# Kernel optimization log

Hardware: AMD Instinct MI355X
Metric: run time of the kernel (lower is better)

Reference implementation:

```python
import jax, jax.numpy as jnp
import numpy as np

W_BIJ, W_ORTH, W_LAP, W_PRE = 1000.0, 1000.0, 1.0, 100000.0
N, V, C, K = 8, 5000, 128, 128
NUM_DESC = int(C * 0.2)  # 25, matches sub_pre=0.2


def setup_inputs() -> dict:
    key = jax.random.key(0)
    ks = jax.random.split(key, 10)
    return {
        "C12": jax.random.normal(ks[0], (N, K, K), jnp.float32) * 0.1,
        "C21": jax.random.normal(ks[1], (N, K, K), jnp.float32) * 0.1,
        "feat_1": jax.random.normal(ks[2], (N, V, C), jnp.float32),
        "feat_2": jax.random.normal(ks[3], (N, V, C), jnp.float32),
        "evecs_1": jax.random.normal(ks[4], (N, V, K), jnp.float32) * 0.02,
        "evecs_2": jax.random.normal(ks[5], (N, V, K), jnp.float32) * 0.02,
        "evecs_trans1": jax.random.normal(ks[6], (N, K, V), jnp.float32) * 0.02,
        "evecs_trans2": jax.random.normal(ks[7], (N, K, V), jnp.float32) * 0.02,
        "evals_1": jax.random.uniform(ks[8], (N, K), jnp.float32),
        "evals_2": jax.random.uniform(ks[9], (N, K), jnp.float32),
        "desc_ind": jnp.arange(NUM_DESC, dtype=jnp.int32),
    }


def _frob3(a, b):
    # torch FrobeniusLoss on [N,K,K]: mean over batch of sum((a-b)^2, dims (1,2))
    return jnp.mean(jnp.sum((a - b) ** 2, axis=(1, 2)))


def reference(C12, C21, feat_1, feat_2, evecs_1, evecs_2,
              evecs_trans1, evecs_trans2, evals_1, evals_2, desc_ind):
    n, k, _ = C12.shape
    eye = jnp.eye(k, dtype=C12.dtype)[None]  # broadcasts over batch

    l_bij = (_frob3(jnp.einsum('nij,njk->nik', C12, C21), eye)
             + _frob3(jnp.einsum('nij,njk->nik', C21, C12), eye)) * W_BIJ

    l_orth = (_frob3(jnp.einsum('nji,njk->nik', C12, C12), eye)
              + _frob3(jnp.einsum('nji,njk->nik', C21, C21), eye)) * W_ORTH

    # diag-scale commutativity: C * evals (col scale) vs evals * C (row scale)
    l_lap = (_frob3(C12 * evals_1[:, None, :], evals_2[:, :, None] * C12)
             + _frob3(C21 * evals_2[:, None, :], evals_1[:, :, None] * C21)) * W_LAP

    # descriptor preservation via commutativity, D = num_desc subsampled channels
    f1 = feat_1[:, :, desc_ind]  # [N,V,D]
    f2 = feat_2[:, :, desc_ind]
    # M[n,d] = Phi_trans @ diag(f[:,d]) @ Phi  (KxK per descriptor), fused einsum
    M1 = jnp.einsum('nkv,nvd,nvj->ndkj', evecs_trans1, f1, evecs_1)
    M2 = jnp.einsum('nkv,nvd,nvj->ndkj', evecs_trans2, f2, evecs_2)
    s1 = jnp.einsum('nij,ndjk->ndik', C12, M1)  # C12 @ M1_d
    t1 = jnp.einsum('ndij,njk->ndik', M2, C12)  # M2_d @ C12
    s2 = jnp.einsum('nij,ndjk->ndik', C21, M2)
    t2 = jnp.einsum('ndij,njk->ndik', M1, C21)
    # torch FrobeniusLoss on 5D [N,D,1,K,K]: sum over axes (1,2), then global mean
    # over remaining [N,K,K] -> total_sum / (N*K*K)
    denom = jnp.asarray(n * k * k, s1.dtype)
    l_pre = ((jnp.sum((s1 - t1) ** 2) + jnp.sum((s2 - t2) ** 2)) / denom) * W_PRE

    return jnp.stack([l_bij, l_orth, l_lap, l_pre])
```

## Files before the change

kernel.cpp:

```cpp
#include <hip/hip_runtime.h>

typedef float v4f __attribute__((ext_vector_type(4)));
typedef unsigned int u32;
typedef __attribute__((ext_vector_type(4))) u32 u32x4;
typedef __attribute__((ext_vector_type(8))) short bhalf8;

#define K 128
#define W_BIJ 1000.0f
#define W_ORTH 1000.0f
#define W_LAP 1.0f
#define W_PRE 100000.0f

#define NCH 79
#define TILE_B 16384
#define CTILE_B 32768
#define VPAD 5120

union B8 { u32x4 u; bhalf8 h; };

static __device__ __forceinline__ unsigned short f2b(float x) {
    union { float f; unsigned int u; } v; v.f = x;
    unsigned int u = v.u + 0x7FFFu + ((v.u >> 16) & 1u);
    return (unsigned short)(u >> 16);
}
static __device__ __forceinline__ u32 pk2(float lo, float hi) {
    return (u32)f2b(lo) | ((u32)f2b(hi) << 16);
}
static __device__ __forceinline__ float bitsf(u32 x) {
    union { u32 u; float f; } v; v.u = x; return v.f;
}
static __device__ __forceinline__ u32 cvtpk(float lo, float hi) {
    u32 r; asm("v_cvt_pk_bf16_f32 %0, %1, %2" : "=v"(r) : "v"(lo), "v"(hi)); return r;
}
static __device__ __forceinline__ void gload_lds16(const void* g, void* l) {
    __builtin_amdgcn_global_load_lds((const __attribute__((address_space(1))) u32*)g,
                                     (__attribute__((address_space(3))) u32*)l, 16, 0, 0);
}

extern "C" __global__ __launch_bounds__(256, 2)
void surfm_conv(const float* __restrict__ T1, const float* __restrict__ T2,
                const float* __restrict__ E1, const float* __restrict__ E2,
                const float* __restrict__ F1, const float* __restrict__ F2,
                const float* __restrict__ C12g, const float* __restrict__ C21g,
                const int* __restrict__ desc,
                unsigned short* __restrict__ Abf, unsigned short* __restrict__ Ebf,
                float* __restrict__ Fbf, char* __restrict__ Cbf,
                int V, int CF)
{
    __shared__ char csm[32768];
    const int b = blockIdx.x;
    const int tid = threadIdx.x;

    if (b < 1264) {
        const int c  = b % NCH;
        const int mn = b / NCH;
        const float* src = ((mn & 8) ? T2 : T1) + (size_t)(mn & 7) * K * V;
        char* dst = (char*)Abf + (size_t)b * TILE_B;
        #pragma unroll
        for (int it = 0; it < 4; ++it) {
            const int item = it * 256 + tid;
            const int grp = item & 7, r = item >> 3;
            const int kg = grp ^ (r & 7);
            const int k = c * 64 + kg * 8;
            u32x4 o = (u32x4){0u,0u,0u,0u};
            if (k + 8 <= V) {
                const v4f lo = *(const v4f*)(src + (size_t)r * V + k);
                const v4f hi = *(const v4f*)(src + (size_t)r * V + k + 4);
                o[0] = pk2(lo[0], lo[1]); o[1] = pk2(lo[2], lo[3]);
                o[2] = pk2(hi[0], hi[1]); o[3] = pk2(hi[2], hi[3]);
            }
            *(u32x4*)(dst + r * 128 + grp * 16) = o;
        }
    } else if (b < 2528) {
        const int idx = b - 1264;
        const int c  = idx % NCH;
        const int mn = idx / NCH;
        const float* src = ((mn & 8) ? E2 : E1) + (size_t)(mn & 7) * V * K;
        char* dst = (char*)Ebf + (size_t)idx * TILE_B;
        #pragma unroll
        for (int it = 0; it < 8; ++it) {
            const int item = it * 256 + tid;
            const int vp = item >> 5;
            const int j4 = (item & 31) * 4;
            const int v = c * 64 + vp * 2;
            v4f e0 = {0.f,0.f,0.f,0.f}, e1 = e0;
            if (v < V)     e0 = *(const v4f*)(src + (size_t)v * K + j4);
            if (v + 1 < V) e1 = *(const v4f*)(src + (size_t)(v + 1) * K + j4);
            #pragma unroll
            for (int e = 0; e < 4; ++e) {
                const int j = j4 + e;
                *(u32*)(csm + j * 128 + vp * 4) = pk2(e0[e], e1[e]);
            }
        }
        __syncthreads();
        #pragma unroll
        for (int it = 0; it < 4; ++it) {
            const int item = it * 256 + tid;
            *(u32x4*)(dst + item * 16) = *(const u32x4*)(csm + item * 16);
        }
    } else if (b < 2928) {
        const int idx = b - 2528;
        const int d  = idx % 25;
        const int mn = idx / 25;
        const int col = desc[d];
        const float* src = ((mn & 8) ? F2 : F1) + (size_t)(mn & 7) * V * CF + col;
        float* dst = Fbf + (size_t)idx * VPAD;
        for (int i = tid; i < VPAD; i += 256)
            dst[i] = (i < V) ? src[(size_t)i * CF] : 0.0f;
    } else {
        const int idx = b - 2928;
        const float* src = ((idx & 8) ? C21g : C12g) + (size_t)(idx & 7) * K * K;
        char* outN = Cbf + (size_t)(idx * 2 + 0) * CTILE_B;
        char* outT = Cbf + (size_t)(idx * 2 + 1) * CTILE_B;
        #pragma unroll
        for (int it = 0; it < 8; ++it) {
            const int item = it * 256 + tid;
            const int r = item >> 4, grp = item & 15;
            const int g = grp ^ (r & 7);
            const v4f lo = *(const v4f*)(src + r * K + g * 8);
            const v4f hi = *(const v4f*)(src + r * K + g * 8 + 4);
            u32x4 o;
            o[0] = pk2(lo[0], lo[1]); o[1] = pk2(lo[2], lo[3]);
            o[2] = pk2(hi[0], hi[1]); o[3] = pk2(hi[2], hi[3]);
            *(u32x4*)(outN + r * 256 + grp * 16) = o;
        }
        #pragma unroll
        for (int it = 0; it < 8; ++it) {
            const int item = it * 256 + tid;
            const int rp = item >> 5;
            const int j4 = (item & 31) * 4;
            const v4f r0 = *(const v4f*)(src + (2 * rp) * K + j4);
            const v4f r1 = *(const v4f*)(src + (2 * rp + 1) * K + j4);
            #pragma unroll
            for (int e = 0; e < 4; ++e) {
                const int j = j4 + e;
                *(u32*)(csm + j * 256 + ((rp * 4) ^ ((j & 7) << 4))) = pk2(r0[e], r1[e]);
            }
        }
        __syncthreads();
        #pragma unroll
        for (int it = 0; it < 8; ++it) {
            const int item = it * 256 + tid;
            *(u32x4*)(outT + item * 16) = *(const u32x4*)(csm + item * 16);
        }
    }
}

extern "C" __global__ __launch_bounds__(512, 4)
void surfm_stage1(const char* __restrict__ Abf, const char* __restrict__ Ebf,
                  const float* __restrict__ Fbf, float* __restrict__ Mpart,
                  int partStride)
{
    extern __shared__ char sm[];
    const int tid = threadIdx.x;
    const int l  = tid & 63;
    const int wv = tid >> 6;
    const int wq = __builtin_amdgcn_readfirstlane(wv);
    const int b = blockIdx.x;
    const int n = b & 7;
    const int vh = (b >> 3) & 1;
    const int rest = b >> 4;
    const int mat = rest & 1;
    const int dgi = rest >> 1;
    const int d0 = dgi * 2;
    const bool hasD1 = (d0 + 1) < 25;

    const int mn = mat * 8 + n;
    const char* gA = Abf + (size_t)mn * NCH * TILE_B;
    const char* gE = Ebf + (size_t)mn * NCH * TILE_B;
    const char* gW = (const char*)(Fbf + ((size_t)mn * 25 + d0) * VPAD) + vh * 10240;

    const int c0 = vh ? 40 : 0;
    const int NT = vh ? 39 : 40;

    const int lm = l & 15;
    const int lk = (l >> 4) * 8;
    const int j  = wq * 16 + lm;
    const int rkey = (lm & 7) << 4;
    float* wLds = (float*)(sm + 32768);

    v4f acc0[8], acc1[8];
    #pragma unroll
    for (int mf = 0; mf < 8; ++mf) {
        acc0[mf] = (v4f){0.f,0.f,0.f,0.f};
        acc1[mf] = (v4f){0.f,0.f,0.f,0.f};
    }

    for (int i = wq; i < 20; i += 8) {
        const int dd = i / 10, off = (i - dd * 10) * 1024;
        gload_lds16(gW + dd * 20480 + off + l * 16, sm + 32768 + dd * 10240 + off);
    }
    {
        const char* t = gA + (size_t)c0 * TILE_B;
        gload_lds16(t + (wq * 2 + 0) * 1024 + l * 16, sm + (wq * 2 + 0) * 1024);
        gload_lds16(t + (wq * 2 + 1) * 1024 + l * 16, sm + (wq * 2 + 1) * 1024);
    }
    const char* gEl = gE + j * 128 + lk * 2;
    u32x4 eC0 = *(const u32x4*)(gEl + (size_t)c0 * TILE_B);
    u32x4 eC1 = *(const u32x4*)(gEl + (size_t)c0 * TILE_B + 64);
    asm volatile("s_waitcnt vmcnt(0)" ::: "memory");
    __builtin_amdgcn_s_barrier();

    #pragma unroll 1
    for (int t = 0; t < NT; ++t) {
        const int par = t & 1;
        u32x4 eN0 = eC0, eN1 = eC1;
        if (t + 1 < NT) {
            const char* tA = gA + (size_t)(c0 + t + 1) * TILE_B;
            char* dA = sm + (par ^ 1) * 16384;
            gload_lds16(tA + (wq * 2 + 0) * 1024 + l * 16, dA + (wq * 2 + 0) * 1024);
            gload_lds16(tA + (wq * 2 + 1) * 1024 + l * 16, dA + (wq * 2 + 1) * 1024);
            const char* tE = gEl + (size_t)(c0 + t + 1) * TILE_B;
            eN0 = *(const u32x4*)(tE);
            eN1 = *(const u32x4*)(tE + 64);
            asm volatile("s_waitcnt vmcnt(4)" ::: "memory");
        } else {
            asm volatile("s_waitcnt vmcnt(0)" ::: "memory");
        }
        __builtin_amdgcn_s_barrier();
        __builtin_amdgcn_sched_barrier(0);

        const char* Ab = sm + par * 16384;
        #pragma unroll
        for (int ks = 0; ks < 2; ++ks) {
            const u32x4 e = ks ? eC1 : eC0;
            const float* pw0 = wLds + t * 64 + ks * 32 + lk;
            const float* pw1 = pw0 + 2560;
            const v4f w0a = *(const v4f*)pw0, w0b = *(const v4f*)(pw0 + 4);
            const v4f w1a = *(const v4f*)pw1, w1b = *(const v4f*)(pw1 + 4);
            const float wl0[4] = {w0a[0], w0a[2], w0b[0], w0b[2]};
            const float wh0[4] = {w0a[1], w0a[3], w0b[1], w0b[3]};
            const float wl1[4] = {w1a[0], w1a[2], w1b[0], w1b[2]};
            const float wh1[4] = {w1a[1], w1a[3], w1b[1], w1b[3]};
            B8 p0, p1;
            #pragma unroll
            for (int t4 = 0; t4 < 4; ++t4) {
                const float elo = bitsf(e[t4] << 16);
                const float ehi = bitsf(e[t4] & 0xFFFF0000u);
                p0.u[t4] = cvtpk(elo * wl0[t4], ehi * wh0[t4]);
                p1.u[t4] = cvtpk(elo * wl1[t4], ehi * wh1[t4]);
            }
            const int kb = ks * 64 + lk * 2;
            #pragma unroll
            for (int mf = 0; mf < 8; ++mf) {
                const int r = mf * 16 + lm;
                B8 a; a.u = *(const u32x4*)(Ab + r * 128 + (kb ^ rkey));
                acc0[mf] = __builtin_amdgcn_mfma_f32_16x16x32_bf16(a.h, p0.h, acc0[mf], 0, 0, 0);
                acc1[mf] = __builtin_amdgcn_mfma_f32_16x16x32_bf16(a.h, p1.h, acc1[mf], 0, 0, 0);
            }
        }
        eC0 = eN0; eC1 = eN1;
        __builtin_amdgcn_s_barrier();
    }

    const int slotM = (n * 25 + d0) * 2 + mat;
    const int rbase = (l >> 4) * 4;
    {
        float* dst = Mpart + ((size_t)(vh * partStride + slotM)) * 16384 + j * 128 + rbase;
        if (partStride) {
            #pragma unroll
            for (int mf = 0; mf < 8; ++mf) *(v4f*)(dst + mf * 16) = acc0[mf];
        } else {
            #pragma unroll
            for (int mf = 0; mf < 8; ++mf)
                #pragma unroll
                for (int e = 0; e < 4; ++e) atomicAdd(dst + mf * 16 + e, acc0[mf][e]);
        }
    }
    if (hasD1) {
        float* dst = Mpart + ((size_t)(vh * partStride + slotM + 2)) * 16384 + j * 128 + rbase;
        if (partStride) {
            #pragma unroll
            for (int mf = 0; mf < 8; ++mf) *(v4f*)(dst + mf * 16) = acc1[mf];
        } else {
            #pragma unroll
            for (int mf = 0; mf < 8; ++mf)
                #pragma unroll
                for (int e = 0; e < 4; ++e) atomicAdd(dst + mf * 16 + e, acc1[mf][e]);
        }
    }
}

extern "C" __global__ __launch_bounds__(256, 2)
void surfm_mconv(const float* __restrict__ Mpart, int nPart,
                 char* __restrict__ Mbf)
{
    extern __shared__ char sm[];
    float* sMT = (float*)sm;
    const int s = blockIdx.x;
    const int tid = threadIdx.x;
    const float* p0 = Mpart + (size_t)s * 16384;
    for (int i = tid; i < 4096; i += 256) {
        const int jj = i >> 5, r4 = (i & 31) * 4;
        v4f v = *(const v4f*)(p0 + jj * 128 + r4);
        if (nPart == 2) v += *(const v4f*)(p0 + (size_t)400 * 16384 + jj * 128 + r4);
        *(v4f*)(sMT + jj * 132 + r4) = v;
    }
    __syncthreads();
    char* outN = Mbf + (size_t)s * 65536;
    char* outT = outN + 32768;
    #pragma unroll
    for (int it = 0; it < 16; ++it) {
        const int item = it * 256 + tid;
        const int lay = item >> 11;
        const int g2 = item & 2047;
        const int rr = g2 >> 4, grp = g2 & 15;
        const int g = grp ^ (rr & 7);
        u32x4 o;
        if (lay == 0) {
            const float* p = sMT + rr * 132 + g * 8;
            const v4f a = *(const v4f*)p, bq = *(const v4f*)(p + 4);
            o[0] = pk2(a[0], a[1]);   o[1] = pk2(a[2], a[3]);
            o[2] = pk2(bq[0], bq[1]); o[3] = pk2(bq[2], bq[3]);
            *(u32x4*)(outT + rr * 256 + grp * 16) = o;
        } else {
            const float* p = sMT + (g * 8) * 132 + rr;
            o[0] = pk2(p[0],   p[132]); o[1] = pk2(p[264], p[396]);
            o[2] = pk2(p[528], p[660]); o[3] = pk2(p[792], p[924]);
            *(u32x4*)(outN + rr * 256 + grp * 16) = o;
        }
    }
}

extern "C" __global__ __launch_bounds__(256, 1)
void surfm_stage2(const float* __restrict__ C12g, const float* __restrict__ C21g,
                  const float* __restrict__ ev1g, const float* __restrict__ ev2g,
                  const char* __restrict__ Cbf, const char* __restrict__ Mbf,
                  float* __restrict__ out, int N, int ND)
{
    extern __shared__ char sm[];
    const int b = blockIdx.x;
    const int tid = threadIdx.x;
    const int nPre = N * ND;

    if (b < nPre) {
        const int n = b & 7, d = b >> 3;
        const size_t slot = n * 25 + d;
        const int l = tid & 63;
        const int wq = __builtin_amdgcn_readfirstlane(tid >> 6);
        const int lm = l & 15, lk = (l >> 4) * 8;
        const int wm = wq >> 1, wj = wq & 1;
        float rsum = 0.0f;

        #pragma unroll 1
        for (int ph = 0; ph < 2; ++ph) {
            const char* s0 = Cbf + ((size_t)(ph * 8 + n) * 2 + 0) * CTILE_B;
            const char* s1 = Mbf + (slot * 2 + (ph ? 1 : 0)) * 65536 + 32768;
            const char* s2 = Mbf + (slot * 2 + (ph ? 0 : 1)) * 65536;
            const char* s3 = Cbf + ((size_t)(ph * 8 + n) * 2 + 1) * CTILE_B;
            const char* gs = (wq == 0) ? s0 : (wq == 1) ? s1 : (wq == 2) ? s2 : s3;
            char* ld = sm + wq * 32768;
            if (ph) __builtin_amdgcn_s_barrier();
            #pragma unroll
            for (int i = 0; i < 32; ++i)
                gload_lds16(gs + i * 1024 + l * 16, ld + i * 1024);
            asm volatile("s_waitcnt vmcnt(0)" ::: "memory");
            __builtin_amdgcn_s_barrier();
            __builtin_amdgcn_sched_barrier(0);

            v4f as_[4][4], at_[4][4];
            #pragma unroll
            for (int mf = 0; mf < 4; ++mf)
                #pragma unroll
                for (int jf = 0; jf < 4; ++jf) {
                    as_[mf][jf] = (v4f){0.f,0.f,0.f,0.f};
                    at_[mf][jf] = (v4f){0.f,0.f,0.f,0.f};
                }
            #pragma unroll
            for (int ks = 0; ks < 4; ++ks) {
                const int kb = ks * 64 + lk * 2;
                B8 bS[4], bT[4];
                #pragma unroll
                for (int jf = 0; jf < 4; ++jf) {
                    const int jj = wj * 64 + jf * 16 + lm;
                    const int off = jj * 256 + (kb ^ ((jj & 7) << 4));
                    bS[jf].u = *(const u32x4*)(sm + 32768 + off);
                    bT[jf].u = *(const u32x4*)(sm + 98304 + off);
                }
                #pragma unroll
                for (int mf = 0; mf < 4; ++mf) {
                    const int r = wm * 64 + mf * 16 + lm;
                    const int off = r * 256 + (kb ^ ((r & 7) << 4));
                    B8 aS; aS.u = *(const u32x4*)(sm + off);
                    B8 aT; aT.u = *(const u32x4*)(sm + 65536 + off);
                    #pragma unroll
                    for (int jf = 0; jf < 4; ++jf) {
                        as_[mf][jf] = __builtin_amdgcn_mfma_f32_16x16x32_bf16(aS.h, bS[jf].h, as_[mf][jf], 0, 0, 0);
                        at_[mf][jf] = __builtin_amdgcn_mfma_f32_16x16x32_bf16(aT.h, bT[jf].h, at_[mf][jf], 0, 0, 0);
                    }
                }
            }
            #pragma unroll
            for (int mf = 0; mf < 4; ++mf)
                #pragma unroll
                for (int jf = 0; jf < 4; ++jf) {
                    const v4f df = as_[mf][jf] - at_[mf][jf];
                    rsum += df[0]*df[0] + df[1]*df[1] + df[2]*df[2] + df[3]*df[3];
                }
        }
        #pragma unroll
        for (int off = 32; off; off >>= 1) rsum += __shfl_down(rsum, off, 64);
        if (l == 0)
            atomicAdd(out + 3, rsum * (W_PRE / (float)(N * K * K)));
    } else {
        float* lds = (float*)sm;
        const int idx = b - nPre;
        const int n = idx >> 2, p = idx & 3;
        const float* c12 = C12g + (size_t)n * K * K;
        const float* c21 = C21g + (size_t)n * K * K;
        const float* Xg = (p == 1 || p == 3) ? c21 : c12;
        const float* Yg = (p == 0) ? c21 : c12;
        const float* ea = (p == 0) ? ev1g + n * K : ev2g + n * K;
        const float* eb = (p == 0) ? ev2g + n * K : ev1g + n * K;
        float* X = lds;
        float* Y = lds + K * 129;
        const int tx = tid & 15, ty = tid >> 4;
        float lap = 0.0f;
        for (int i = tid; i < K * K / 4; i += 256) {
            const int r = i >> 5, c4 = (i & 31) * 4;
            const v4f x = *(const v4f*)(Xg + r * K + c4);
            X[r * 129 + c4 + 0] = x[0]; X[r * 129 + c4 + 1] = x[1];
            X[r * 129 + c4 + 2] = x[2]; X[r * 129 + c4 + 3] = x[3];
            if (p < 2) {
                const v4f y = *(const v4f*)(Yg + r * K + c4);
                Y[r * 129 + c4 + 0] = y[0]; Y[r * 129 + c4 + 1] = y[1];
                Y[r * 129 + c4 + 2] = y[2]; Y[r * 129 + c4 + 3] = y[3];
                const float ebi = eb[r];
                #pragma unroll
                for (int e = 0; e < 4; ++e) {
                    const float dlt = ea[c4 + e] - ebi;
                    lap += x[e] * x[e] * dlt * dlt;
                }
            }
        }
        __syncthreads();
        const int i0 = ty * 8, k0 = tx * 8;
        float z[8][8];
        #pragma unroll
        for (int i = 0; i < 8; ++i)
            #pragma unroll
            for (int t = 0; t < 8; ++t) z[i][t] = 0.0f;
        for (int jj = 0; jj < K; ++jj) {
            float xi[8], yk[8];
            if (p < 2) {
                #pragma unroll
                for (int i = 0; i < 8; ++i) xi[i] = X[(i0 + i) * 129 + jj];
                #pragma unroll
                for (int t = 0; t < 8; ++t) yk[t] = Y[jj * 129 + k0 + t];
            } else {
// ... 177 lines not shown
        v4f acc1a[8], acc1b[8], acc2a[8], acc2b[8];
        #pragma unroll
        for (int i = 0; i < 8; ++i) {
            acc1a[i] = (v4f){0,0,0,0}; acc1b[i] = (v4f){0,0,0,0};
            acc2a[i] = (v4f){0,0,0,0}; acc2b[i] = (v4f){0,0,0,0};
        }
        for (int jj = 0; jj < K; ++jj) {
            const int keyj = (jj >> 3) & 7;
            const int ga = (tx ^ keyj) << 2;
            const int gb = ((16 + tx) ^ keyj) << 2;
            const v4f m1ra = *(const v4f*)(M1 + jj * K + ga);
            const v4f m1rb = *(const v4f*)(M1 + jj * K + gb);
            const v4f m2ra = *(const v4f*)(M2 + jj * K + ga);
            const v4f m2rb = *(const v4f*)(M2 + jj * K + gb);
            const v4f c12ra = *(const v4f*)(c12 + jj * K + ca);
            const v4f c12rb = *(const v4f*)(c12 + jj * K + cb);
            const v4f c21ra = *(const v4f*)(c21 + jj * K + ca);
            const v4f c21rb = *(const v4f*)(c21 + jj * K + cb);
            const int jp = (((jj >> 2) ^ kcol) << 2) | (jj & 3);
            #pragma unroll
            for (int i = 0; i < 8; ++i) {
                const int r = r0 + i;
                const float x12 = c12[r * K + jj];
                const float x21 = c21[r * K + jj];
                const float m1c = M1[r * K + jp];
                const float m2c = M2[r * K + jp];
                acc1a[i] += m1ra * x12; acc1a[i] -= c12ra * m2c;
                acc1b[i] += m1rb * x12; acc1b[i] -= c12rb * m2c;
                acc2a[i] += m2ra * x21; acc2a[i] -= c21ra * m1c;
                acc2b[i] += m2rb * x21; acc2b[i] -= c21rb * m1c;
            }
        }
        float s = 0.0f;
        #pragma unroll
        for (int i = 0; i < 8; ++i)
            #pragma unroll
            for (int e = 0; e < 4; ++e) {
                s += acc1a[i][e] * acc1a[i][e] + acc1b[i][e] * acc1b[i][e];
                s += acc2a[i][e] * acc2a[i][e] + acc2b[i][e] * acc2b[i][e];
            }
        #pragma unroll
        for (int off = 32; off; off >>= 1) s += __shfl_down(s, off, 64);
        if ((tid & 63) == 0)
            atomicAdd(out + 3, s * (W_PRE / (float)(N * K * K)));
    } else {
        float* ldsf = (float*)smem;
        const int idx = b - nPre;
        const int n = idx >> 2, p = idx & 3;
        const float* c12 = C12g + (size_t)n * K * K;
        const float* c21 = C21g + (size_t)n * K * K;
        const float* Xg = (p == 1 || p == 3) ? c21 : c12;
        const float* Yg = (p == 0) ? c21 : c12;
        const float* ea = (p == 0) ? ev1g + n * K : ev2g + n * K;
        const float* eb = (p == 0) ? ev2g + n * K : ev1g + n * K;
        float* X = ldsf;
        float* Y = ldsf + K * 129;
        const int tx = tid & 15, ty = tid >> 4;
        float lap = 0.0f;
        for (int i = tid; i < K * K / 4; i += 256) {
            const int r = i >> 5, c4 = (i & 31) * 4;
            const v4f x = *(const v4f*)(Xg + r * K + c4);
            X[r * 129 + c4 + 0] = x[0]; X[r * 129 + c4 + 1] = x[1];
            X[r * 129 + c4 + 2] = x[2]; X[r * 129 + c4 + 3] = x[3];
            if (p < 2) {
                const v4f y = *(const v4f*)(Yg + r * K + c4);
                Y[r * 129 + c4 + 0] = y[0]; Y[r * 129 + c4 + 1] = y[1];
                Y[r * 129 + c4 + 2] = y[2]; Y[r * 129 + c4 + 3] = y[3];
                const float ebi = eb[r];
                #pragma unroll
                for (int e = 0; e < 4; ++e) {
                    const float dlt = ea[c4 + e] - ebi;
                    lap += x[e] * x[e] * dlt * dlt;
                }
            }
        }
        __syncthreads();
        const int i0 = ty * 8, k0 = tx * 8;
        float z[8][8];
        #pragma unroll
        for (int i = 0; i < 8; ++i)
            #pragma unroll
            for (int t = 0; t < 8; ++t) z[i][t] = 0.0f;
        for (int jj = 0; jj < K; ++jj) {
            float xi[8], yk[8];
            if (p < 2) {
                #pragma unroll
                for (int i = 0; i < 8; ++i) xi[i] = X[(i0 + i) * 129 + jj];
                #pragma unroll
                for (int t = 0; t < 8; ++t) yk[t] = Y[jj * 129 + k0 + t];
            } else {
                #pragma unroll
                for (int i = 0; i < 8; ++i) xi[i] = X[jj * 129 + i0 + i];
                #pragma unroll
                for (int t = 0; t < 8; ++t) yk[t] = X[jj * 129 + k0 + t];
            }
            #pragma unroll
            for (int i = 0; i < 8; ++i)
                #pragma unroll
                for (int t = 0; t < 8; ++t) z[i][t] += xi[i] * yk[t];
        }
        float s = 0.0f;
        #pragma unroll
        for (int i = 0; i < 8; ++i)
            #pragma unroll
            for (int t = 0; t < 8; ++t) {
                const float e = z[i][t] - ((i0 + i) == (k0 + t) ? 1.0f : 0.0f);
                s += e * e;
            }
        #pragma unroll
        for (int off = 32; off; off >>= 1) {
            s   += __shfl_down(s, off, 64);
            lap += __shfl_down(lap, off, 64);
        }
        if ((tid & 63) == 0) {
            if (p < 2) {
                atomicAdd(out + 0, s * (W_BIJ / (float)N));
                atomicAdd(out + 2, lap * (W_LAP / (float)N));
            } else {
                atomicAdd(out + 1, s * (W_ORTH / (float)N));
            }
        }
    }
}

extern "C" void kernel_launch(void* const* d_in, const int* in_sizes, int n_in,
                              void* d_out, int out_size, void* d_ws, size_t ws_size,
                              hipStream_t stream) {
    (void)n_in;
    const float* C12 = (const float*)d_in[0];
    const float* C21 = (const float*)d_in[1];
    const float* F1  = (const float*)d_in[2];
    const float* F2  = (const float*)d_in[3];
    const float* E1  = (const float*)d_in[4];
    const float* E2  = (const float*)d_in[5];
    const float* T1  = (const float*)d_in[6];
    const float* T2  = (const float*)d_in[7];
    const float* ev1 = (const float*)d_in[8];
    const float* ev2 = (const float*)d_in[9];
    const int* desc  = (const int*)d_in[10];
    float* out = (float*)d_out;

    const int N  = in_sizes[8] / K;
    const int ND = in_sizes[10];
    const int V  = in_sizes[4] / (N * K);
    const int CF = in_sizes[2] / (N * V);

    hipMemsetAsync(d_out, 0, (size_t)out_size * sizeof(float), stream);

    const size_t ABF = (size_t)16 * NCH * TILE_B;
    const size_t EBF = ABF;
    const size_t FBF = (size_t)400 * VPAD * 4;
    const size_t CBF = (size_t)32 * CTILE_B;
    const size_t MBF = (size_t)400 * 65536;
    const size_t MP1 = (size_t)400 * 65536;
    const size_t base = ABF + EBF + FBF + CBF + MBF;
    const size_t needPart   = base + 2 * MP1;
    const size_t needAtomic = base + 1 * MP1;

    const bool okShape = (N == 8 && ND == 25 && V == 5000 && CF == 128);
    int mode = 0;
    if (okShape && ws_size >= needPart) mode = 2;
    else if (okShape && ws_size >= needAtomic) mode = 1;

    if (mode == 0) {
        const size_t shmem = (size_t)(2 * K * 129) * sizeof(float);
        hipFuncSetAttribute((const void*)surfm_fused,
                            hipFuncAttributeMaxDynamicSharedMemorySize, (int)shmem);
        const int blocks = N * ND + 4 * N;
        surfm_fused<<<blocks, 256, shmem, stream>>>(C12, C21, F1, F2, E1, E2, T1, T2,
                                                    ev1, ev2, desc, out, N, ND, V, CF);
        return;
    }

    char* ws = (char*)d_ws;
    unsigned short* Abf = (unsigned short*)ws;
    unsigned short* Ebf = (unsigned short*)(ws + ABF);
    float* Fbf = (float*)(ws + ABF + EBF);
    char* Cbf = ws + ABF + EBF + FBF;
    char* Mbf = ws + ABF + EBF + FBF + CBF;
    float* Mpart = (float*)(ws + base);

    surfm_conv<<<2944, 256, 0, stream>>>(T1, T2, E1, E2, F1, F2, C12, C21, desc,
                                         Abf, Ebf, Fbf, Cbf, V, CF);

    if (mode == 1)
        hipMemsetAsync(Mpart, 0, MP1, stream);

    const size_t shmem1 = 53248;
    hipFuncSetAttribute((const void*)surfm_stage1,
                        hipFuncAttributeMaxDynamicSharedMemorySize, (int)shmem1);
    surfm_stage1<<<416, 512, shmem1, stream>>>((const char*)Abf, (const char*)Ebf,
                                               Fbf, Mpart, (mode == 2) ? 400 : 0);

    const size_t shmemM = (size_t)128 * 132 * 4;
    hipFuncSetAttribute((const void*)surfm_mconv,
                        hipFuncAttributeMaxDynamicSharedMemorySize, (int)shmemM);
    surfm_mconv<<<400, 256, shmemM, stream>>>(Mpart, (mode == 2) ? 2 : 1, Mbf);

    const size_t shmem2 = 132096;
    hipFuncSetAttribute((const void*)surfm_stage2,
                        hipFuncAttributeMaxDynamicSharedMemorySize, (int)shmem2);
    surfm_stage2<<<N * ND + 4 * N, 256, shmem2, stream>>>(C12, C21, ev1, ev2,
                                                          Cbf, Mbf, out, N, ND);
}
```

Measured before the change: 187.6 us.

## Switch stage1 to 32x32x16 MFMA with row-split blocks and coalesced feature gather

Stage1 now uses 32x32x16 bf16 MFMA fragments with 256-thread blocks. Each block covers half of the K rows, which doubles the grid to 832 blocks and shrinks LDS per block. The A-matrix conversion now writes a k-major layout through LDS to match the new fragment reads. The descriptor gather now reads whole feature rows coalesced into LDS and picks the selected columns, instead of strided per-column loads. The atomic fallback mode is dropped, so the split-partials path is always used when workspace allows. The intent is better MFMA efficiency, occupancy and gather bandwidth, at the cost of E fragments being loaded redundantly by both row halves.

```diff
diff --git a/kernel.cpp b/kernel.cpp
--- a/kernel.cpp
+++ b/kernel.cpp
@@ -1,6 +1,7 @@
 #include <hip/hip_runtime.h>
 
 typedef float v4f __attribute__((ext_vector_type(4)));
+typedef __attribute__((ext_vector_type(16))) float v16f;
 typedef unsigned int u32;
 typedef __attribute__((ext_vector_type(4))) u32 u32x4;
 typedef __attribute__((ext_vector_type(8))) short bhalf8;
@@ -47,7 +48,7 @@
                 float* __restrict__ Fbf, char* __restrict__ Cbf,
                 int V, int CF)
 {
-    __shared__ char csm[32768];
+    __shared__ char csm[36992];
     const int b = blockIdx.x;
     const int tid = threadIdx.x;
 
@@ -59,9 +60,8 @@
         #pragma unroll
         for (int it = 0; it < 4; ++it) {
             const int item = it * 256 + tid;
-            const int grp = item & 7, r = item >> 3;
-            const int kg = grp ^ (r & 7);
-            const int k = c * 64 + kg * 8;
+            const int r = item >> 3, ko = item & 7;
+            const int k = c * 64 + ko * 8;
             u32x4 o = (u32x4){0u,0u,0u,0u};
             if (k + 8 <= V) {
                 const v4f lo = *(const v4f*)(src + (size_t)r * V + k);
@@ -69,7 +69,13 @@
                 o[0] = pk2(lo[0], lo[1]); o[1] = pk2(lo[2], lo[3]);
                 o[2] = pk2(hi[0], hi[1]); o[3] = pk2(hi[2], hi[3]);
             }
-            *(u32x4*)(dst + r * 128 + grp * 16) = o;
+            *(u32x4*)(csm + ko * 2048 + r * 16) = o;
+        }
+        __syncthreads();
+        #pragma unroll
+        for (int it = 0; it < 4; ++it) {
+            const int item = it * 256 + tid;
+            *(u32x4*)(dst + item * 16) = *(const u32x4*)(csm + item * 16);
         }
     } else if (b < 2528) {
         const int idx = b - 1264;
@@ -98,17 +104,38 @@
             const int item = it * 256 + tid;
             *(u32x4*)(dst + item * 16) = *(const u32x4*)(csm + item * 16);
         }
-    } else if (b < 2928) {
+    } else if (b < 2688) {
         const int idx = b - 2528;
-        const int d  = idx % 25;
-        const int mn = idx / 25;
-        const int col = desc[d];
-        const float* src = ((mn & 8) ? F2 : F1) + (size_t)(mn & 7) * V * CF + col;
-        float* dst = Fbf + (size_t)idx * VPAD;
-        for (int i = tid; i < VPAD; i += 256)
-            dst[i] = (i < V) ? src[(size_t)i * CF] : 0.0f;
+        const int vc = idx % 10;
+        const int mn = idx / 10;
+        const float* src = ((mn & 8) ? F2 : F1) + (size_t)(mn & 7) * V * CF;
+        float* dstB = Fbf + (size_t)(mn * 25) * VPAD + vc * 512;
+        int* sdesc = (int*)csm;
+        float* stg = (float*)(csm + 128);
+        if (tid < 25) sdesc[tid] = desc[tid];
+        #pragma unroll 1
+        for (int pass = 0; pass < 8; ++pass) {
+            const int vbase = vc * 512 + pass * 64;
+            __syncthreads();
+            #pragma unroll
+            for (int it = 0; it < 8; ++it) {
+                const int item = it * 256 + tid;
+                const int vloc = item >> 5;
+                const int c4 = (item & 31) * 4;
+                const int v = vbase + vloc;
+                v4f x = {0.f,0.f,0.f,0.f};
+                if (v < V) x = *(const v4f*)(src + (size_t)v * CF + c4);
+                float* p = stg + vloc * 129 + c4;
+                p[0] = x[0]; p[1] = x[1]; p[2] = x[2]; p[3] = x[3];
+            }
+            __syncthreads();
+            for (int i = tid; i < 1600; i += 256) {
+                const int d = i >> 6, vloc = i & 63;
+                dstB[(size_t)d * VPAD + pass * 64 + vloc] = stg[vloc * 129 + sdesc[d]];
+            }
+        }
     } else {
-        const int idx = b - 2928;
+        const int idx = b - 2688;
         const float* src = ((idx & 8) ? C21g : C12g) + (size_t)(idx & 7) * K * K;
         char* outN = Cbf + (size_t)(idx * 2 + 0) * CTILE_B;
         char* outT = Cbf + (size_t)(idx * 2 + 1) * CTILE_B;
@@ -146,7 +173,7 @@
     }
 }
 
-extern "C" __global__ __launch_bounds__(512, 4)
+extern "C" __global__ __launch_bounds__(256, 3)
 void surfm_stage1(const char* __restrict__ Abf, const char* __restrict__ Ebf,
                   const float* __restrict__ Fbf, float* __restrict__ Mpart,
                   int partStride)
@@ -154,14 +181,13 @@
     extern __shared__ char sm[];
     const int tid = threadIdx.x;
     const int l  = tid & 63;
-    const int wv = tid >> 6;
-    const int wq = __builtin_amdgcn_readfirstlane(wv);
+    const int wq = __builtin_amdgcn_readfirstlane(tid >> 6);
     const int b = blockIdx.x;
-    const int n = b & 7;
-    const int vh = (b >> 3) & 1;
-    const int rest = b >> 4;
-    const int mat = rest & 1;
-    const int dgi = rest >> 1;
+    const int n   = b & 7;
+    const int mh  = (b >> 3) & 1;
+    const int vh  = (b >> 4) & 1;
+    const int mat = (b >> 5) & 1;
+    const int dgi = b >> 6;
     const int d0 = dgi * 2;
     const bool hasD1 = (d0 + 1) < 25;
 
@@ -169,62 +195,62 @@
     const char* gA = Abf + (size_t)mn * NCH * TILE_B;
     const char* gE = Ebf + (size_t)mn * NCH * TILE_B;
     const char* gW = (const char*)(Fbf + ((size_t)mn * 25 + d0) * VPAD) + vh * 10240;
-
     const int c0 = vh ? 40 : 0;
     const int NT = vh ? 39 : 40;
 
-    const int lm = l & 15;
-    const int lk = (l >> 4) * 8;
-    const int j  = wq * 16 + lm;
-    const int rkey = (lm & 7) << 4;
-    float* wLds = (float*)(sm + 32768);
-
-    v4f acc0[8], acc1[8];
+    const int lj = l & 31;
+    const int lh = l >> 5;
+    const int j  = wq * 32 + lj;
+    const int aBase = lh * 1024 + lj * 16;
+    float* wLds = (float*)(sm + 16384);
+
+    v16f acc[2][2];
     #pragma unroll
-    for (int mf = 0; mf < 8; ++mf) {
-        acc0[mf] = (v4f){0.f,0.f,0.f,0.f};
-        acc1[mf] = (v4f){0.f,0.f,0.f,0.f};
-    }
-
-    for (int i = wq; i < 20; i += 8) {
-        const int dd = i / 10, off = (i - dd * 10) * 1024;
-        gload_lds16(gW + dd * 20480 + off + l * 16, sm + 32768 + dd * 10240 + off);
-    }
+    for (int dd = 0; dd < 2; ++dd)
+        #pragma unroll
+        for (int mf = 0; mf < 2; ++mf)
+            #pragma unroll
+            for (int q = 0; q < 16; ++q) acc[dd][mf][q] = 0.0f;
+
+    for (int i = wq; i < 20; i += 4)
+        gload_lds16(gW + i * 1024 + l * 16, sm + 16384 + i * 1024);
     {
-        const char* t = gA + (size_t)c0 * TILE_B;
-        gload_lds16(t + (wq * 2 + 0) * 1024 + l * 16, sm + (wq * 2 + 0) * 1024);
-        gload_lds16(t + (wq * 2 + 1) * 1024 + l * 16, sm + (wq * 2 + 1) * 1024);
-    }
-    const char* gEl = gE + j * 128 + lk * 2;
-    u32x4 eC0 = *(const u32x4*)(gEl + (size_t)c0 * TILE_B);
-    u32x4 eC1 = *(const u32x4*)(gEl + (size_t)c0 * TILE_B + 64);
+        const char* t = gA + (size_t)c0 * TILE_B + mh * 1024;
+        gload_lds16(t + (wq * 2 + 0) * 2048 + l * 16, sm + (wq * 2 + 0) * 1024);
+        gload_lds16(t + (wq * 2 + 1) * 2048 + l * 16, sm + (wq * 2 + 1) * 1024);
+    }
+    const char* gEl = gE + j * 128 + lh * 16;
+    u32x4 eC[4], eN[4];
+    {
+        const char* s = gEl + (size_t)c0 * TILE_B;
+        #pragma unroll
+        for (int ks = 0; ks < 4; ++ks) eC[ks] = *(const u32x4*)(s + ks * 32);
+    }
     asm volatile("s_waitcnt vmcnt(0)" ::: "memory");
     __builtin_amdgcn_s_barrier();
 
     #pragma unroll 1
     for (int t = 0; t < NT; ++t) {
         const int par = t & 1;
-        u32x4 eN0 = eC0, eN1 = eC1;
         if (t + 1 < NT) {
-            const char* tA = gA + (size_t)(c0 + t + 1) * TILE_B;
-            char* dA = sm + (par ^ 1) * 16384;
-            gload_lds16(tA + (wq * 2 + 0) * 1024 + l * 16, dA + (wq * 2 + 0) * 1024);
-            gload_lds16(tA + (wq * 2 + 1) * 1024 + l * 16, dA + (wq * 2 + 1) * 1024);
+            const char* tA = gA + (size_t)(c0 + t + 1) * TILE_B + mh * 1024;
+            char* dA = sm + (par ^ 1) * 8192;
+            gload_lds16(tA + (wq * 2 + 0) * 2048 + l * 16, dA + (wq * 2 + 0) * 1024);
+            gload_lds16(tA + (wq * 2 + 1) * 2048 + l * 16, dA + (wq * 2 + 1) * 1024);
             const char* tE = gEl + (size_t)(c0 + t + 1) * TILE_B;
-            eN0 = *(const u32x4*)(tE);
-            eN1 = *(const u32x4*)(tE + 64);
-            asm volatile("s_waitcnt vmcnt(4)" ::: "memory");
+            #pragma unroll
+            for (int ks = 0; ks < 4; ++ks) eN[ks] = *(const u32x4*)(tE + ks * 32);
+            asm volatile("s_waitcnt vmcnt(6)" ::: "memory");
         } else {
             asm volatile("s_waitcnt vmcnt(0)" ::: "memory");
         }
         __builtin_amdgcn_s_barrier();
         __builtin_amdgcn_sched_barrier(0);
 
-        const char* Ab = sm + par * 16384;
-        #pragma unroll
-        for (int ks = 0; ks < 2; ++ks) {
-            const u32x4 e = ks ? eC1 : eC0;
-            const float* pw0 = wLds + t * 64 + ks * 32 + lk;
+        const char* Ab = sm + par * 8192;
+        #pragma unroll
+        for (int ks = 0; ks < 4; ++ks) {
+            const float* pw0 = wLds + t * 64 + ks * 16 + lh * 8;
             const float* pw1 = pw0 + 2560;
             const v4f w0a = *(const v4f*)pw0, w0b = *(const v4f*)(pw0 + 4);
             const v4f w1a = *(const v4f*)pw1, w1b = *(const v4f*)(pw1 + 4);
@@ -234,50 +260,42 @@
             const float wh1[4] = {w1a[1], w1a[3], w1b[1], w1b[3]};
             B8 p0, p1;
             #pragma unroll
-            for (int t4 = 0; t4 < 4; ++t4) {
-                const float elo = bitsf(e[t4] << 16);
-                const float ehi = bitsf(e[t4] & 0xFFFF0000u);
-                p0.u[t4] = cvtpk(elo * wl0[t4], ehi * wh0[t4]);
-                p1.u[t4] = cvtpk(elo * wl1[t4], ehi * wh1[t4]);
-            }
-            const int kb = ks * 64 + lk * 2;
-            #pragma unroll
-            for (int mf = 0; mf < 8; ++mf) {
-                const int r = mf * 16 + lm;
-                B8 a; a.u = *(const u32x4*)(Ab + r * 128 + (kb ^ rkey));
-                acc0[mf] = __builtin_amdgcn_mfma_f32_16x16x32_bf16(a.h, p0.h, acc0[mf], 0, 0, 0);
-                acc1[mf] = __builtin_amdgcn_mfma_f32_16x16x32_bf16(a.h, p1.h, acc1[mf], 0, 0, 0);
-            }
-        }
-        eC0 = eN0; eC1 = eN1;
+            for (int q = 0; q < 4; ++q) {
+                const float elo = bitsf(eC[ks][q] << 16);
+                const float ehi = bitsf(eC[ks][q] & 0xFFFF0000u);
+                p0.u[q] = cvtpk(elo * wl0[q], ehi * wh0[q]);
+                p1.u[q] = cvtpk(elo * wl1[q], ehi * wh1[q]);
+            }
+            B8 a0, a1;
+            a0.u = *(const u32x4*)(Ab + aBase + ks * 2048);
+            a1.u = *(const u32x4*)(Ab + aBase + ks * 2048 + 512);
+            acc[0][0] = __builtin_amdgcn_mfma_f32_32x32x16_bf16(a0.h, p0.h, acc[0][0], 0, 0, 0);
+            acc[0][1] = __builtin_amdgcn_mfma_f32_32x32x16_bf16(a1.h, p0.h, acc[0][1], 0, 0, 0);
+            acc[1][0] = __builtin_amdgcn_mfma_f32_32x32x16_bf16(a0.h, p1.h, acc[1][0], 0, 0, 0);
+            acc[1][1] = __builtin_amdgcn_mfma_f32_32x32x16_bf16(a1.h, p1.h, acc[1][1], 0, 0, 0);
+        }
+        #pragma unroll
+        for (int ks = 0; ks < 4; ++ks) eC[ks] = eN[ks];
         __builtin_amdgcn_s_barrier();
     }
 
-    const int slotM = (n * 25 + d0) * 2 + mat;
-    const int rbase = (l >> 4) * 4;
-    {
-        float* dst = Mpart + ((size_t)(vh * partStride + slotM)) * 16384 + j * 128 + rbase;
-        if (partStride) {
-            #pragma unroll
-            for (int mf = 0; mf < 8; ++mf) *(v4f*)(dst + mf * 16) = acc0[mf];
-        } else {
-            #pragma unroll
-            for (int mf = 0; mf < 8; ++mf)
-                #pragma unroll
-                for (int e = 0; e < 4; ++e) atomicAdd(dst + mf * 16 + e, acc0[mf][e]);
-        }
-    }
-    if (hasD1) {
-        float* dst = Mpart + ((size_t)(vh * partStride + slotM + 2)) * 16384 + j * 128 + rbase;
-        if (partStride) {
-            #pragma unroll
-            for (int mf = 0; mf < 8; ++mf) *(v4f*)(dst + mf * 16) = acc1[mf];
-        } else {
-            #pragma unroll
-            for (int mf = 0; mf < 8; ++mf)
-                #pragma unroll
-                for (int e = 0; e < 4; ++e) atomicAdd(dst + mf * 16 + e, acc1[mf][e]);
-        }
+    const int slotBase = (n * 25 + d0) * 2 + mat;
+    const int r0 = mh * 64 + 4 * lh;
+    #pragma unroll
+    for (int dd = 0; dd < 2; ++dd) {
+        if (dd == 1 && !hasD1) break;
+        float* dst = Mpart + ((size_t)(vh * partStride + slotBase + dd * 2)) * 16384 + j * 128;
+        #pragma unroll
+        for (int mf = 0; mf < 2; ++mf)
+            #pragma unroll
+            for (int tq = 0; tq < 4; ++tq) {
+                v4f v;
+                v[0] = acc[dd][mf][4 * tq + 0];
+                v[1] = acc[dd][mf][4 * tq + 1];
+                v[2] = acc[dd][mf][4 * tq + 2];
+                v[3] = acc[dd][mf][4 * tq + 3];
+                *(v4f*)(dst + r0 + mf * 32 + 8 * tq) = v;
+            }
     }
 }
 
@@ -780,15 +798,10 @@
     const size_t MBF = (size_t)400 * 65536;
     const size_t MP1 = (size_t)400 * 65536;
     const size_t base = ABF + EBF + FBF + CBF + MBF;
-    const size_t needPart   = base + 2 * MP1;
-    const size_t needAtomic = base + 1 * MP1;
+    const size_t needPart = base + 2 * MP1;
 
     const bool okShape = (N == 8 && ND == 25 && V == 5000 && CF == 128);
-    int mode = 0;
-    if (okShape && ws_size >= needPart) mode = 2;
-    else if (okShape && ws_size >= needAtomic) mode = 1;
-
-    if (mode == 0) {
+    if (!okShape || ws_size < needPart) {
         const size_t shmem = (size_t)(2 * K * 129) * sizeof(float);
         hipFuncSetAttribute((const void*)surfm_fused,
                             hipFuncAttributeMaxDynamicSharedMemorySize, (int)shmem);
@@ -806,22 +819,19 @@
     char* Mbf = ws + ABF + EBF + FBF + CBF;
     float* Mpart = (float*)(ws + base);
 
-    surfm_conv<<<2944, 256, 0, stream>>>(T1, T2, E1, E2, F1, F2, C12, C21, desc,
+    surfm_conv<<<2704, 256, 0, stream>>>(T1, T2, E1, E2, F1, F2, C12, C21, desc,
                                          Abf, Ebf, Fbf, Cbf, V, CF);
 
-    if (mode == 1)
-        hipMemsetAsync(Mpart, 0, MP1, stream);
-
-    const size_t shmem1 = 53248;
+    const size_t shmem1 = 36864;
     hipFuncSetAttribute((const void*)surfm_stage1,
                         hipFuncAttributeMaxDynamicSharedMemorySize, (int)shmem1);
-    surfm_stage1<<<416, 512, shmem1, stream>>>((const char*)Abf, (const char*)Ebf,
-                                               Fbf, Mpart, (mode == 2) ? 400 : 0);
+    surfm_stage1<<<832, 256, shmem1, stream>>>((const char*)Abf, (const char*)Ebf,
+                                               Fbf, Mpart, 400);
 
     const size_t shmemM = (size_t)128 * 132 * 4;
     hipFuncSetAttribute((const void*)surfm_mconv,
                         hipFuncAttributeMaxDynamicSharedMemorySize, (int)shmemM);
-    surfm_mconv<<<400, 256, shmemM, stream>>>(Mpart, (mode == 2) ? 2 : 1, Mbf);
+    surfm_mconv<<<400, 256, shmemM, stream>>>(Mpart, 2, Mbf);
 
     const size_t shmem2 = 132096;
     hipFuncSetAttribute((const void*)surfm_stage2,
```

New measurement: 233.0 us. 1.24x slower.

## Split stage1 V range into quarters with bf16 partials and coalesced feature gather

Applied to the files above, without the earlier changes.

Stage1 now splits the vertex dimension into four chunks instead of two, doubling the grid to 832 blocks for better CU occupancy. It writes bf16 partial M tiles instead of fp32, and mconv sums the four partials. The feature-column gather is reworked so each block loads contiguous rows into LDS and then extracts the descriptor columns, replacing strided scalar loads. The second MFMA is also skipped when the block has no second descriptor. The cost is extra partial traffic and a bf16 rounding of partial sums before the reduction, which may affect accuracy.

```diff
diff --git a/kernel.cpp b/kernel.cpp
--- a/kernel.cpp
+++ b/kernel.cpp
@@ -2,6 +2,7 @@
 
 typedef float v4f __attribute__((ext_vector_type(4)));
 typedef unsigned int u32;
+typedef __attribute__((ext_vector_type(2))) u32 u32x2;
 typedef __attribute__((ext_vector_type(4))) u32 u32x4;
 typedef __attribute__((ext_vector_type(8))) short bhalf8;
 
@@ -47,7 +48,7 @@
                 float* __restrict__ Fbf, char* __restrict__ Cbf,
                 int V, int CF)
 {
-    __shared__ char csm[32768];
+    __shared__ char csm[36992];
     const int b = blockIdx.x;
     const int tid = threadIdx.x;
 
@@ -98,17 +99,38 @@
             const int item = it * 256 + tid;
             *(u32x4*)(dst + item * 16) = *(const u32x4*)(csm + item * 16);
         }
-    } else if (b < 2928) {
+    } else if (b < 2688) {
         const int idx = b - 2528;
-        const int d  = idx % 25;
-        const int mn = idx / 25;
-        const int col = desc[d];
-        const float* src = ((mn & 8) ? F2 : F1) + (size_t)(mn & 7) * V * CF + col;
-        float* dst = Fbf + (size_t)idx * VPAD;
-        for (int i = tid; i < VPAD; i += 256)
-            dst[i] = (i < V) ? src[(size_t)i * CF] : 0.0f;
+        const int vc = idx % 10;
+        const int mn = idx / 10;
+        const float* src = ((mn & 8) ? F2 : F1) + (size_t)(mn & 7) * V * CF;
+        float* dstB = Fbf + (size_t)(mn * 25) * VPAD + vc * 512;
+        int* sdesc = (int*)csm;
+        float* stg = (float*)(csm + 128);
+        if (tid < 25) sdesc[tid] = desc[tid];
+        #pragma unroll 1
+        for (int pass = 0; pass < 8; ++pass) {
+            const int vbase = vc * 512 + pass * 64;
+            __syncthreads();
+            #pragma unroll
+            for (int it = 0; it < 8; ++it) {
+                const int item = it * 256 + tid;
+                const int vloc = item >> 5;
+                const int c4 = (item & 31) * 4;
+                const int v = vbase + vloc;
+                v4f x = {0.f,0.f,0.f,0.f};
+                if (v < V) x = *(const v4f*)(src + (size_t)v * CF + c4);
+                float* p = stg + vloc * 129 + c4;
+                p[0] = x[0]; p[1] = x[1]; p[2] = x[2]; p[3] = x[3];
+            }
+            __syncthreads();
+            for (int i = tid; i < 1600; i += 256) {
+                const int d = i >> 6, vloc = i & 63;
+                dstB[(size_t)d * VPAD + pass * 64 + vloc] = stg[vloc * 129 + sdesc[d]];
+            }
+        }
     } else {
-        const int idx = b - 2928;
+        const int idx = b - 2688;
         const float* src = ((idx & 8) ? C21g : C12g) + (size_t)(idx & 7) * K * K;
         char* outN = Cbf + (size_t)(idx * 2 + 0) * CTILE_B;
         char* outT = Cbf + (size_t)(idx * 2 + 1) * CTILE_B;
@@ -148,30 +170,27 @@
 
 extern "C" __global__ __launch_bounds__(512, 4)
 void surfm_stage1(const char* __restrict__ Abf, const char* __restrict__ Ebf,
-                  const float* __restrict__ Fbf, float* __restrict__ Mpart,
-                  int partStride)
+                  const float* __restrict__ Fbf, char* __restrict__ MpartB)
 {
     extern __shared__ char sm[];
     const int tid = threadIdx.x;
     const int l  = tid & 63;
-    const int wv = tid >> 6;
-    const int wq = __builtin_amdgcn_readfirstlane(wv);
+    const int wq = __builtin_amdgcn_readfirstlane(tid >> 6);
     const int b = blockIdx.x;
     const int n = b & 7;
-    const int vh = (b >> 3) & 1;
-    const int rest = b >> 4;
+    const int rest = b >> 3;
     const int mat = rest & 1;
-    const int dgi = rest >> 1;
+    const int vq  = (rest >> 1) & 3;
+    const int dgi = rest >> 3;
     const int d0 = dgi * 2;
     const bool hasD1 = (d0 + 1) < 25;
 
     const int mn = mat * 8 + n;
     const char* gA = Abf + (size_t)mn * NCH * TILE_B;
     const char* gE = Ebf + (size_t)mn * NCH * TILE_B;
-    const char* gW = (const char*)(Fbf + ((size_t)mn * 25 + d0) * VPAD) + vh * 10240;
-
-    const int c0 = vh ? 40 : 0;
-    const int NT = vh ? 39 : 40;
+    const char* gW = (const char*)(Fbf + ((size_t)mn * 25 + d0) * VPAD) + vq * 5120;
+    const int c0 = vq * 20;
+    const int NT = (vq == 3) ? 19 : 20;
 
     const int lm = l & 15;
     const int lk = (l >> 4) * 8;
@@ -186,10 +205,9 @@
         acc1[mf] = (v4f){0.f,0.f,0.f,0.f};
     }
 
-    for (int i = wq; i < 20; i += 8) {
-        const int dd = i / 10, off = (i - dd * 10) * 1024;
-        gload_lds16(gW + dd * 20480 + off + l * 16, sm + 32768 + dd * 10240 + off);
-    }
+    for (int i = wq; i < 10; i += 8)
+        gload_lds16(gW + (i / 5) * (VPAD * 4) + (i % 5) * 1024 + l * 16,
+                    sm + 32768 + (i / 5) * 5120 + (i % 5) * 1024);
     {
         const char* t = gA + (size_t)c0 * TILE_B;
         gload_lds16(t + (wq * 2 + 0) * 1024 + l * 16, sm + (wq * 2 + 0) * 1024);
@@ -225,7 +243,7 @@
         for (int ks = 0; ks < 2; ++ks) {
             const u32x4 e = ks ? eC1 : eC0;
             const float* pw0 = wLds + t * 64 + ks * 32 + lk;
-            const float* pw1 = pw0 + 2560;
+            const float* pw1 = pw0 + 1280;
             const v4f w0a = *(const v4f*)pw0, w0b = *(const v4f*)(pw0 + 4);
             const v4f w1a = *(const v4f*)pw1, w1b = *(const v4f*)(pw1 + 4);
             const float wl0[4] = {w0a[0], w0a[2], w0b[0], w0b[2]};
@@ -238,7 +256,7 @@
                 const float elo = bitsf(e[t4] << 16);
                 const float ehi = bitsf(e[t4] & 0xFFFF0000u);
                 p0.u[t4] = cvtpk(elo * wl0[t4], ehi * wh0[t4]);
-                p1.u[t4] = cvtpk(elo * wl1[t4], ehi * wh1[t4]);
+                if (hasD1) p1.u[t4] = cvtpk(elo * wl1[t4], ehi * wh1[t4]);
             }
             const int kb = ks * 64 + lk * 2;
             #pragma unroll
@@ -246,7 +264,8 @@
                 const int r = mf * 16 + lm;
                 B8 a; a.u = *(const u32x4*)(Ab + r * 128 + (kb ^ rkey));
                 acc0[mf] = __builtin_amdgcn_mfma_f32_16x16x32_bf16(a.h, p0.h, acc0[mf], 0, 0, 0);
-                acc1[mf] = __builtin_amdgcn_mfma_f32_16x16x32_bf16(a.h, p1.h, acc1[mf], 0, 0, 0);
+                if (hasD1)
+                    acc1[mf] = __builtin_amdgcn_mfma_f32_16x16x32_bf16(a.h, p1.h, acc1[mf], 0, 0, 0);
             }
         }
         eC0 = eN0; eC1 = eN1;
@@ -254,47 +273,52 @@
     }
 
     const int slotM = (n * 25 + d0) * 2 + mat;
-    const int rbase = (l >> 4) * 4;
+    const int rbyte = (l >> 4) * 8;
     {
-        float* dst = Mpart + ((size_t)(vh * partStride + slotM)) * 16384 + j * 128 + rbase;
-        if (partStride) {
-            #pragma unroll
-            for (int mf = 0; mf < 8; ++mf) *(v4f*)(dst + mf * 16) = acc0[mf];
-        } else {
-            #pragma unroll
-            for (int mf = 0; mf < 8; ++mf)
-                #pragma unroll
-                for (int e = 0; e < 4; ++e) atomicAdd(dst + mf * 16 + e, acc0[mf][e]);
+        char* dst = MpartB + ((size_t)(vq * 400 + slotM)) * 32768 + j * 256 + rbyte;
+        #pragma unroll
+        for (int mf = 0; mf < 8; ++mf) {
+            u32x2 o;
+            o[0] = pk2(acc0[mf][0], acc0[mf][1]);
+            o[1] = pk2(acc0[mf][2], acc0[mf][3]);
+            *(u32x2*)(dst + mf * 32) = o;
         }
     }
     if (hasD1) {
-        float* dst = Mpart + ((size_t)(vh * partStride + slotM + 2)) * 16384 + j * 128 + rbase;
-        if (partStride) {
-            #pragma unroll
-            for (int mf = 0; mf < 8; ++mf) *(v4f*)(dst + mf * 16) = acc1[mf];
-        } else {
-            #pragma unroll
-            for (int mf = 0; mf < 8; ++mf)
-                #pragma unroll
-                for (int e = 0; e < 4; ++e) atomicAdd(dst + mf * 16 + e, acc1[mf][e]);
+        char* dst = MpartB + ((size_t)(vq * 400 + slotM + 2)) * 32768 + j * 256 + rbyte;
+        #pragma unroll
+        for (int mf = 0; mf < 8; ++mf) {
+            u32x2 o;
+            o[0] = pk2(acc1[mf][0], acc1[mf][1]);
+            o[1] = pk2(acc1[mf][2], acc1[mf][3]);
+            *(u32x2*)(dst + mf * 32) = o;
         }
     }
 }
 
 extern "C" __global__ __launch_bounds__(256, 2)
-void surfm_mconv(const float* __restrict__ Mpart, int nPart,
-                 char* __restrict__ Mbf)
+void surfm_mconv(const char* __restrict__ MpartB, char* __restrict__ Mbf)
 {
     extern __shared__ char sm[];
     float* sMT = (float*)sm;
     const int s = blockIdx.x;
     const int tid = threadIdx.x;
-    const float* p0 = Mpart + (size_t)s * 16384;
-    for (int i = tid; i < 4096; i += 256) {
-        const int jj = i >> 5, r4 = (i & 31) * 4;
-        v4f v = *(const v4f*)(p0 + jj * 128 + r4);
-        if (nPart == 2) v += *(const v4f*)(p0 + (size_t)400 * 16384 + jj * 128 + r4);
-        *(v4f*)(sMT + jj * 132 + r4) = v;
+    const char* p0 = MpartB + (size_t)s * 32768;
+    for (int i = tid; i < 2048; i += 256) {
+        const int jj = i >> 4, g = i & 15;
+        float sum[8] = {0.f,0.f,0.f,0.f,0.f,0.f,0.f,0.f};
+        #pragma unroll
+        for (int p = 0; p < 4; ++p) {
+            const u32x4 v = *(const u32x4*)(p0 + (size_t)p * 400 * 32768 + jj * 256 + g * 16);
+            #pragma unroll
+            for (int e = 0; e < 4; ++e) {
+                sum[2 * e + 0] += bitsf(v[e] << 16);
+                sum[2 * e + 1] += bitsf(v[e] & 0xFFFF0000u);
+            }
+        }
+        float* q = sMT + jj * 132 + g * 8;
+        #pragma unroll
+        for (int e = 0; e < 8; ++e) q[e] = sum[e];
     }
     __syncthreads();
     char* outN = Mbf + (size_t)s * 65536;
@@ -778,17 +802,12 @@
     const size_t FBF = (size_t)400 * VPAD * 4;
     const size_t CBF = (size_t)32 * CTILE_B;
     const size_t MBF = (size_t)400 * 65536;
-    const size_t MP1 = (size_t)400 * 65536;
+    const size_t MPB = (size_t)4 * 400 * 32768;
     const size_t base = ABF + EBF + FBF + CBF + MBF;
-    const size_t needPart   = base + 2 * MP1;
-    const size_t needAtomic = base + 1 * MP1;
+    const size_t needPart = base + MPB;
 
     const bool okShape = (N == 8 && ND == 25 && V == 5000 && CF == 128);
-    int mode = 0;
-    if (okShape && ws_size >= needPart) mode = 2;
-    else if (okShape && ws_size >= needAtomic) mode = 1;
-
-    if (mode == 0) {
+    if (!okShape || ws_size < needPart) {
         const size_t shmem = (size_t)(2 * K * 129) * sizeof(float);
         hipFuncSetAttribute((const void*)surfm_fused,
                             hipFuncAttributeMaxDynamicSharedMemorySize, (int)shmem);
@@ -804,24 +823,21 @@
     float* Fbf = (float*)(ws + ABF + EBF);
     char* Cbf = ws + ABF + EBF + FBF;
     char* Mbf = ws + ABF + EBF + FBF + CBF;
-    float* Mpart = (float*)(ws + base);
-
-    surfm_conv<<<2944, 256, 0, stream>>>(T1, T2, E1, E2, F1, F2, C12, C21, desc,
+    char* MpartB = ws + base;
+
+    surfm_conv<<<2704, 256, 0, stream>>>(T1, T2, E1, E2, F1, F2, C12, C21, desc,
                                          Abf, Ebf, Fbf, Cbf, V, CF);
 
-    if (mode == 1)
-        hipMemsetAsync(Mpart, 0, MP1, stream);
-
-    const size_t shmem1 = 53248;
+    const size_t shmem1 = 43008;
     hipFuncSetAttribute((const void*)surfm_stage1,
                         hipFuncAttributeMaxDynamicSharedMemorySize, (int)shmem1);
-    surfm_stage1<<<416, 512, shmem1, stream>>>((const char*)Abf, (const char*)Ebf,
-                                               Fbf, Mpart, (mode == 2) ? 400 : 0);
+    surfm_stage1<<<832, 512, shmem1, stream>>>((const char*)Abf, (const char*)Ebf,
+                                               Fbf, MpartB);
 
     const size_t shmemM = (size_t)128 * 132 * 4;
     hipFuncSetAttribute((const void*)surfm_mconv,
                         hipFuncAttributeMaxDynamicSharedMemorySize, (int)shmemM);
-    surfm_mconv<<<400, 256, shmemM, stream>>>(Mpart, (mode == 2) ? 2 : 1, Mbf);
+    surfm_mconv<<<400, 256, shmemM, stream>>>(MpartB, Mbf);
 
     const size_t shmem2 = 132096;
     hipFuncSetAttribute((const void*)surfm_stage2,
```

New measurement: 212.3 us. +13.2%, slower.
